# Performance work log

Measured on AMD Instinct MI355X. Metric: run time of the kernel, lower is better.

The kernel has to match this reference:

```python
import jax, jax.numpy as jnp
import numpy as np

DIM_M = 512
NEG_INF = -1e30


def setup_inputs() -> dict:
    key = jax.random.key(0)
    k1, k2, k3, k4, k5, k6, k7 = jax.random.split(key, 7)
    B, Lc, Lq, d = 16, 1024, 512, DIM_M
    C = jax.random.normal(k1, (B, Lc, d), dtype=jnp.float32)
    Q = jax.random.normal(k2, (B, Lq, d), dtype=jnp.float32)
    cmask = jax.random.randint(k3, (B, Lc), 0, 2).astype(jnp.float32)
    qmask = jax.random.randint(k4, (B, Lq), 0, 2).astype(jnp.float32)
    lim = np.sqrt(1.0 / d)
    w = jax.random.uniform(k5, (3 * d,), minval=-lim, maxval=lim, dtype=jnp.float32)
    # out_linear: Linear(4d -> d), torch default init
    bound = np.sqrt(1.0 / (4 * d))
    out_w = jax.random.uniform(k6, (d, 4 * d), minval=-bound, maxval=bound, dtype=jnp.float32)
    out_b = jax.random.uniform(k7, (d,), minval=-bound, maxval=bound, dtype=jnp.float32)
    return {"C": C, "Q": Q, "cmask": cmask, "qmask": qmask, "w": w, "out_w": out_w, "out_b": out_b}


def _mask_logits(t, m):
    return t * m + (1.0 - m) * NEG_INF


def reference(C, Q, cmask, qmask, w, out_w, out_b):
    d = C.shape[-1]
    w1, w2, w3 = w[:d], w[d:2 * d], w[2 * d:]
    # Decomposed trilinear similarity (same math as cat([Ct,Qt,Ct*Qt]) @ w):
    # S[b,i,j] = C[b,i]@w1 + Q[b,j]@w2 + (C[b,i]*w3) @ Q[b,j]
    S = (C @ w1)[:, :, None] + (Q @ w2)[:, None, :] \
        + jnp.einsum('bid,bjd->bij', C * w3, Q)  # [B, Lc, Lq]
    qm = qmask[:, None, :]  # [B, 1, Lq]
    cm = cmask[:, :, None]  # [B, Lc, 1]
    S1 = jax.nn.softmax(_mask_logits(S, qm), axis=2)  # over Lq
    S2 = jax.nn.softmax(_mask_logits(S, cm), axis=1)  # over Lc
    A = jnp.einsum('bij,bjd->bid', S1, Q)  # [B, Lc, d]
    # bmm(bmm(S1, S2^T), C) == S1 @ (S2^T @ C) by associativity (cheaper)
    S2TC = jnp.einsum('bij,bid->bjd', S2, C)  # [B, Lq, d]
    Bm = jnp.einsum('bij,bjd->bid', S1, S2TC)  # [B, Lc, d]
    out = jnp.concatenate([C, A, C * A, C * Bm], axis=2)  # [B, Lc, 4d]
    # dropout inactive (inference); out_linear
    return out @ out_w.T + out_b
```

## Files before the change

kernel.cpp:

```cpp
#include <hip/hip_runtime.h>
#include <hip/hip_bf16.h>


#define NB 16
#define LC 1024
#define LQ 512
#define DM 512
#define D4 2048
#define NEGINF (-1e30f)

typedef __bf16 v8bf __attribute__((ext_vector_type(8)));
typedef __bf16 v4bf __attribute__((ext_vector_type(4)));
typedef float  v4f  __attribute__((ext_vector_type(4)));

#define MFMA16 __builtin_amdgcn_mfma_f32_16x16x32_bf16

#define GLOAD16(gp, lp) __builtin_amdgcn_global_load_lds( \
    (const __attribute__((address_space(1))) void*)(gp), \
    (__attribute__((address_space(3))) void*)(lp), 16, 0, 0)

#define GEMM_PROLOG \
  __shared__ __bf16 Al[2][128 * 64], Bl[2][128 * 64]; \
  int bx = blockIdx.x, by = blockIdx.y, bz = blockIdx.z; \
  xcd_remap(bx, by, bz); \
  const int b = bz, i0 = by * 128, n0 = bx * 128; \
  const int t = threadIdx.x, lane = t & 63, wave = t >> 6; \
  const int wm = wave >> 1, wn = wave & 1, quad = lane >> 4, col = lane & 15; \
  const int srow = wave * 32 + (lane >> 3), scol = (lane & 7) * 8; \
  v4f acc[4][4]; \
  _Pragma("unroll") for (int x = 0; x < 4; ++x) \
  _Pragma("unroll") for (int y = 0; y < 4; ++y) \
  _Pragma("unroll") for (int r = 0; r < 4; ++r) acc[x][y][r] = 0.f;

#define GEMM_STAGE(buf, Aptr, Bptr, LDGA, LDGB, k0) \
  do { _Pragma("unroll") for (int u = 0; u < 4; ++u) { \
    GLOAD16((Aptr) + (size_t)(u * 8) * (LDGA) + (k0), &Al[buf][(wave * 32 + u * 8) * 64]); \
    GLOAD16((Bptr) + (size_t)(u * 8) * (LDGB) + (k0), &Bl[buf][(wave * 32 + u * 8) * 64]); \
  } } while (0)

#define GEMM_COMPUTE(buf) \
  do { _Pragma("unroll") for (int ko = 0; ko < 2; ++ko) { \
    v8bf af_[4], bf_[4]; \
    _Pragma("unroll") for (int x = 0; x < 4; ++x) \
      af_[x] = *(const v8bf*)&Al[buf][(wm * 64 + x * 16 + col) * 64 + ko * 32 + quad * 8]; \
    _Pragma("unroll") for (int y = 0; y < 4; ++y) \
      bf_[y] = *(const v8bf*)&Bl[buf][(wn * 64 + y * 16 + col) * 64 + ko * 32 + quad * 8]; \
    _Pragma("unroll") for (int x = 0; x < 4; ++x) \
    _Pragma("unroll") for (int y = 0; y < 4; ++y) \
      acc[x][y] = MFMA16(af_[x], bf_[y], acc[x][y], 0, 0, 0); \
  } } while (0)

#define GEMM_SYNC() \
  do { asm volatile("s_waitcnt vmcnt(0)" ::: "memory"); \
       __builtin_amdgcn_s_barrier(); } while (0)

#define GEMM_KLOOP(Arow, Brow, LDGA, LDGB, KEXT) \
  { GEMM_STAGE(0, Arow, Brow, LDGA, LDGB, 0); \
    GEMM_SYNC(); \
    int cur_ = 0; \
    for (int k0 = 0; k0 < (KEXT); k0 += 64) { \
      const int kn_ = k0 + 64; \
      if (kn_ < (KEXT)) GEMM_STAGE(cur_ ^ 1, Arow, Brow, LDGA, LDGB, kn_); \
      GEMM_COMPUTE(cur_); \
      GEMM_SYNC(); \
      cur_ ^= 1; \
    } }

__device__ __forceinline__ void xcd_remap(int& bx, int& by, int& bz) {
  const int gx = gridDim.x, gy = gridDim.y, gz = gridDim.z;
  int flat = bx + gx * (by + gy * bz);
  int per = (gx * gy * gz) >> 3;
  int nw = (flat & 7) * per + (flat >> 3);
  bx = nw % gx;
  int r = nw / gx;
  by = r % gy;
  bz = r / gy;
}

__global__ void k_rowdots(const float* __restrict__ C, const float* __restrict__ Q,
                          const float* __restrict__ w,
                          float* __restrict__ cw1, float* __restrict__ qw2,
                          __bf16* __restrict__ Cbf, __bf16* __restrict__ Qw3) {
  const int wid = threadIdx.x >> 6, lane = threadIdx.x & 63;
  const int row = blockIdx.x * 4 + wid;
  const bool isC = row < NB * LC;
  const int lr = isC ? row : row - NB * LC;
  const float* src = (isC ? C : Q) + (size_t)lr * DM;
  const float* wv  = isC ? w : (w + DM);
  const float* w3  = w + 2 * DM;
  __bf16* dst = (isC ? Cbf : Qw3) + (size_t)lr * DM;
  float v = 0.f;
#pragma unroll
  for (int s = 0; s < 2; ++s) {
    const int k = lane * 4 + s * 256;
    float4 f = *(const float4*)(src + k);
    float4 g = *(const float4*)(wv + k);
    v += f.x * g.x + f.y * g.y + f.z * g.z + f.w * g.w;
    v4bf h;
    if (isC) {
      h[0] = (__bf16)f.x; h[1] = (__bf16)f.y; h[2] = (__bf16)f.z; h[3] = (__bf16)f.w;
    } else {
      float4 s3 = *(const float4*)(w3 + k);
      h[0] = (__bf16)(f.x * s3.x); h[1] = (__bf16)(f.y * s3.y);
      h[2] = (__bf16)(f.z * s3.z); h[3] = (__bf16)(f.w * s3.w);
    }
    *(v4bf*)(dst + k) = h;
  }
#pragma unroll
  for (int off = 32; off; off >>= 1) v += __shfl_down(v, off, 64);
  if (lane == 0) {
    if (isC) cw1[row] = v;
    else     qw2[lr] = v;
  }
}

__global__ void k_transpose(const float* __restrict__ in, __bf16* __restrict__ outT,
                            int R, int Cd) {
  __shared__ __bf16 tile[64][66];
  const int b = blockIdx.z;
  const int r0 = blockIdx.y * 64, c0 = blockIdx.x * 64;
  const int tr = threadIdx.x >> 6, tc = threadIdx.x & 63;
  const float* inb = in + (size_t)b * R * Cd;
  __bf16* outb = outT + (size_t)b * Cd * R;
  for (int r = tr; r < 64; r += 4)
    tile[r][tc] = (__bf16)inb[(size_t)(r0 + r) * Cd + c0 + tc];
  __syncthreads();
  for (int c = tr; c < 64; c += 4)
    outb[(size_t)(c0 + c) * R + r0 + tc] = tile[tc][c];
}

__global__ void k_cvt2(const float* __restrict__ Cf, const float* __restrict__ OW,
                       __bf16* __restrict__ Cb3, __bf16* __restrict__ OWb) {
  const size_t NC = (size_t)NB * LC * DM;
  size_t i = ((size_t)blockIdx.x * 256 + threadIdx.x) * 4;
  const float* src; __bf16* dst; size_t j;
  if (i < NC) { src = Cf; dst = Cb3; j = i; }
  else        { src = OW; dst = OWb; j = i - NC; }
  float4 f = *(const float4*)(src + j);
  v4bf h; h[0] = (__bf16)f.x; h[1] = (__bf16)f.y; h[2] = (__bf16)f.z; h[3] = (__bf16)f.w;
  *(v4bf*)(dst + j) = h;
}

__global__ __launch_bounds__(256) void k_mfma_S(
    const __bf16* __restrict__ Cbf, const __bf16* __restrict__ Qw3,
    const float* __restrict__ cw1, const float* __restrict__ qw2,
    float* __restrict__ S) {
  GEMM_PROLOG
  const __bf16* Arow = Cbf + (size_t)b * LC * DM + (size_t)(i0 + srow) * DM + scol;
  const __bf16* Brow = Qw3 + (size_t)b * LQ * DM + (size_t)(n0 + srow) * DM + scol;
  GEMM_KLOOP(Arow, Brow, DM, DM, DM)
  float* Sb = S + (size_t)b * LC * LQ;
#pragma unroll
  for (int x = 0; x < 4; ++x) {
    const int mB = i0 + wm * 64 + x * 16 + quad * 4;
    float cv[4];
#pragma unroll
    for (int r = 0; r < 4; ++r) cv[r] = cw1[b * LC + mB + r];
#pragma unroll
    for (int y = 0; y < 4; ++y) {
      const int j = n0 + wn * 64 + y * 16 + col;
      const float qv = qw2[b * LQ + j];
#pragma unroll
      for (int r = 0; r < 4; ++r)
        Sb[(size_t)(mB + r) * LQ + j] = acc[x][y][r] + cv[r] + qv;
    }
  }
}

__global__ __launch_bounds__(1024) void k_softstat(
    const float* __restrict__ S, const float* __restrict__ qmask,
    const float* __restrict__ cmask, __bf16* __restrict__ S1,
    float2* __restrict__ pstat) {
  __shared__ float2 cst[16][LQ];
  const int b = blockIdx.y, ic = blockIdx.x;
  const int tid = threadIdx.x, wv = tid >> 6, lane = tid & 63;
  const float* qm  = qmask + b * LQ;
  const float* cm  = cmask + b * LC + ic * 64;
  const float* Sb  = S  + ((size_t)b * LC + ic * 64) * LQ;
  __bf16*      S1b = S1 + ((size_t)b * LC + ic * 64) * LQ;
  float colm[8], cols[8];
#pragma unroll
  for (int tt = 0; tt < 8; ++tt) { colm[tt] = -3e38f; cols[tt] = 0.f; }
  for (int it = 0; it < 4; ++it) {
    const int r = wv * 4 + it;
    const float cmv = cm[r];
    const float* Srow = Sb + (size_t)r * LQ;
    float sv[8], l1[8];
    float m = -3e38f;
#pragma unroll
    for (int tt = 0; tt < 8; ++tt) {
      int j = lane + 64 * tt;
      sv[tt] = Srow[j];
      float qv = qm[j];
      l1[tt] = qv * sv[tt] + (1.f - qv) * NEGINF;
      m = fmaxf(m, l1[tt]);
    }
#pragma unroll
    for (int off = 32; off; off >>= 1) m = fmaxf(m, __shfl_xor(m, off, 64));
    float e[8], s = 0.f;
#pragma unroll
    for (int tt = 0; tt < 8; ++tt) { e[tt] = __expf(l1[tt] - m); s += e[tt]; }
#pragma unroll
    for (int off = 32; off; off >>= 1) s += __shfl_xor(s, off, 64);
    const float inv = 1.f / s;
#pragma unroll
    for (int tt = 0; tt < 8; ++tt)
      S1b[(size_t)r * LQ + lane + 64 * tt] = (__bf16)(e[tt] * inv);
    if (cmv != 0.f) {
#pragma unroll
      for (int tt = 0; tt < 8; ++tt) {
        float l2 = sv[tt];
        if (l2 > colm[tt]) { cols[tt] *= __expf(colm[tt] - l2); colm[tt] = l2; }
        cols[tt] += __expf(l2 - colm[tt]);
      }
    }
  }
#pragma unroll
  for (int tt = 0; tt < 8; ++tt) cst[wv][lane + 64 * tt] = make_float2(colm[tt], cols[tt]);
  __syncthreads();
  if (tid < LQ) {
    float M = -3e38f, Sd = 0.f;
#pragma unroll
    for (int k = 0; k < 16; ++k) {
      float2 p = cst[k][tid];
      float nM = fmaxf(M, p.x);
      Sd = Sd * __expf(M - nM) + p.y * __expf(p.x - nM);
      M = nM;
    }
    pstat[((size_t)(b * 16 + ic) * LQ) + tid] = make_float2(M, Sd);
  }
}

__global__ void k_colwrite(const float* __restrict__ S, const float* __restrict__ cmask,
                           const float2* __restrict__ pstat, __bf16* __restrict__ S2T) {
  __shared__ float Mf[64], If[64];
  __shared__ __bf16 tile[64][66];
  const int b = blockIdx.z, ic = blockIdx.y, j0 = blockIdx.x * 64;
  const int c = threadIdx.x & 63, ip = threadIdx.x >> 6;
  if (threadIdx.x < 64) {
    float M = -3e38f, Sd = 0.f;
#pragma unroll
    for (int k = 0; k < 16; ++k) {
      float2 p = pstat[((size_t)(b * 16 + k) * LQ) + j0 + threadIdx.x];
      float nM = fmaxf(M, p.x);
      Sd = Sd * __expf(M - nM) + p.y * __expf(p.x - nM);
      M = nM;
    }
    Mf[threadIdx.x] = M; If[threadIdx.x] = 1.f / Sd;
  }
  __syncthreads();
  const float M = Mf[c], inv = If[c];
  const float* Sb = S + ((size_t)b * LC + ic * 64) * LQ;
  const float* cm = cmask + b * LC + ic * 64;
  for (int r = ip; r < 64; r += 4) {
    if (cm[r] != 0.f)
      tile[r][c] = (__bf16)(__expf(Sb[(size_t)r * LQ + j0 + c] - M) * inv);
    else
      tile[r][c] = (__bf16)0.f;
  }
  __syncthreads();
  __bf16* S2Tb = S2T + ((size_t)b * LQ + j0) * LC + ic * 64;
  for (int jr = ip; jr < 64; jr += 4)
    S2Tb[(size_t)jr * LC + c] = tile[c][jr];
}

__global__ __launch_bounds__(256) void k_mfma_A(
    const __bf16* __restrict__ S1, const __bf16* __restrict__ QT,
    const float* __restrict__ Cf, __bf16* __restrict__ Aw, __bf16* __restrict__ CAw) {
  GEMM_PROLOG
  const __bf16* Arow = S1 + (size_t)b * LC * LQ + (size_t)(i0 + srow) * LQ + scol;
  const __bf16* Brow = QT + (size_t)b * DM * LQ + (size_t)(n0 + srow) * LQ + scol;
  GEMM_KLOOP(Arow, Brow, LQ, LQ, LQ)
  const float* Cb = Cf + (size_t)b * LC * DM;
  __bf16* Ab  = Aw  + (size_t)b * LC * DM;
  __bf16* CAb = CAw + (size_t)b * LC * DM;
#pragma unroll
  for (int x = 0; x < 4; ++x) {
    const int mB = i0 + wm * 64 + x * 16 + quad * 4;
#pragma unroll
    for (int y = 0; y < 4; ++y) {
      const int n = n0 + wn * 64 + y * 16 + col;
#pragma unroll
      for (int r = 0; r < 4; ++r) {
        const float av = acc[x][y][r];
        const float cv = Cb[(size_t)(mB + r) * DM + n];
        Ab[(size_t)(mB + r) * DM + n]  = (__bf16)av;
        CAb[(size_t)(mB + r) * DM + n] = (__bf16)(av * cv);
      }
    }
  }
}

__global__ __launch_bounds__(256) void k_mfma_T(
    const __bf16* __restrict__ S2T, const __bf16* __restrict__ CT, __bf16* __restrict__ S2TCT) {
  GEMM_PROLOG
  const int j0 = i0;
  const __bf16* Arow = S2T + (size_t)b * LQ * LC + (size_t)(j0 + srow) * LC + scol;
  const __bf16* Brow = CT  + (size_t)b * DM * LC + (size_t)(n0 + srow) * LC + scol;
  GEMM_KLOOP(Arow, Brow, LC, LC, LC)
#pragma unroll
  for (int x = 0; x < 4; ++x) {
    const int jB = j0 + wm * 64 + x * 16 + quad * 4;
#pragma unroll
    for (int y = 0; y < 4; ++y) {
      const int n = n0 + wn * 64 + y * 16 + col;
      v4bf h;
#pragma unroll
      for (int r = 0; r < 4; ++r) h[r] = (__bf16)acc[x][y][r];
      *(v4bf*)&S2TCT[((size_t)b * DM + n) * LQ + jB] = h;
    }
  }
}

__global__ __launch_bounds__(256) void k_mfma_Bm(
    const __bf16* __restrict__ S1, const __bf16* __restrict__ S2TCT,
    const float* __restrict__ Cf, __bf16* __restrict__ CBw) {
  GEMM_PROLOG
  const __bf16* Arow = S1    + (size_t)b * LC * LQ + (size_t)(i0 + srow) * LQ + scol;
  const __bf16* Brow = S2TCT + (size_t)b * DM * LQ + (size_t)(n0 + srow) * LQ + scol;
  GEMM_KLOOP(Arow, Brow, LQ, LQ, LQ)
  const float* Cb = Cf + (size_t)b * LC * DM;
  __bf16* CBb = CBw + (size_t)b * LC * DM;
#pragma unroll
  for (int x = 0; x < 4; ++x) {
    const int mB = i0 + wm * 64 + x * 16 + quad * 4;
#pragma unroll
    for (int y = 0; y < 4; ++y) {
      const int n = n0 + wn * 64 + y * 16 + col;
#pragma unroll
      for (int r = 0; r < 4; ++r) {
        const float cv = Cb[(size_t)(mB + r) * DM + n];
        CBb[(size_t)(mB + r) * DM + n] = (__bf16)(acc[x][y][r] * cv);
      }
    }
  }
}

__global__ __launch_bounds__(256) void k_mfma_out(
    const __bf16* __restrict__ Cb3, const __bf16* __restrict__ Aw,
    const __bf16* __restrict__ CAw, const __bf16* __restrict__ CBw,
    const __bf16* __restrict__ OWb, const float* __restrict__ ob,
    float* __restrict__ out) {
  GEMM_PROLOG
  const size_t rowoff = (size_t)b * LC * DM + (size_t)(i0 + srow) * DM + scol;
  const __bf16* As0 = Cb3 + rowoff;
  const __bf16* As1 = Aw  + rowoff;
  const __bf16* As2 = CAw + rowoff;
  const __bf16* As3 = CBw + rowoff;
  const __bf16* Brow0 = OWb + (size_t)(n0 + srow) * D4 + scol;
  GEMM_STAGE(0, As0, Brow0, DM, D4, 0);
  GEMM_SYNC();
  int cur_ = 0;
#pragma unroll
  for (int seg = 0; seg < 4; ++seg) {
    const __bf16* Arow  = (seg == 0) ? As0 : (seg == 1) ? As1 : (seg == 2) ? As2 : As3;
    const __bf16* Anext = (seg == 0) ? As1 : (seg == 1) ? As2 : As3;
    const __bf16* Brow  = Brow0 + seg * DM;
    const __bf16* Bnext = Brow0 + (seg < 3 ? seg + 1 : 3) * DM;
    for (int k0 = 0; k0 < DM; k0 += 64) {
      const int kn_ = k0 + 64;
      if (kn_ < DM)      GEMM_STAGE(cur_ ^ 1, Arow, Brow, DM, D4, kn_);
      else if (seg < 3)  GEMM_STAGE(cur_ ^ 1, Anext, Bnext, DM, D4, 0);
      GEMM_COMPUTE(cur_);
      GEMM_SYNC();
      cur_ ^= 1;
    }
  }
  float* outb = out + (size_t)b * LC * DM;
#pragma unroll
  for (int x = 0; x < 4; ++x) {
    const int mB = i0 + wm * 64 + x * 16 + quad * 4;
#pragma unroll
    for (int y = 0; y < 4; ++y) {
      const int n = n0 + wn * 64 + y * 16 + col;
      const float bv = ob[n];
#pragma unroll
      for (int r = 0; r < 4; ++r)
        outb[(size_t)(mB + r) * DM + n] = acc[x][y][r] + bv;
    }
  }
}

extern "C" void kernel_launch(void* const* d_in, const int* in_sizes, int n_in,
                              void* d_out, int out_size, void* d_ws, size_t ws_size,
                              hipStream_t stream) {
  const float* C     = (const float*)d_in[0];
  const float* Q     = (const float*)d_in[1];
  const float* cmask = (const float*)d_in[2];
  const float* qmask = (const float*)d_in[3];
  const float* w     = (const float*)d_in[4];
  const float* out_w = (const float*)d_in[5];
  const float* out_b = (const float*)d_in[6];
  float* out = (float*)d_out;

  char* base = (char*)d_ws;
  float*  cw1   = (float*)base;
  float*  qw2   = (float*)(base + 65536);
  char*   R     = base + 131072;
  float*  S     = (float*)R;
  __bf16* CT    = (__bf16*)R;
  __bf16* Aw    = (__bf16*)R;
  __bf16* QT    = (__bf16*)(R + (16u << 20));
  __bf16* CBw   = (__bf16*)(R + (16u << 20));
  __bf16* Cbf_e = (__bf16*)(R + (32u << 20));
  __bf16* S1    = (__bf16*)(R + (32u << 20));
  __bf16* Cbf3  = (__bf16*)(R + (32u << 20));
  __bf16* Qw3   = (__bf16*)(R + (48u << 20));
  __bf16* S2T   = (__bf16*)(R + (48u << 20));
  __bf16* CAw   = (__bf16*)(R + (48u << 20));
  float2* pstat = (float2*)(R + (64u << 20));
  __bf16* S2TCT = (__bf16*)(R + (64u << 20));
  __bf16* OWbf  = (__bf16*)(R + (64u << 20));
  (void)in_sizes; (void)n_in; (void)out_size; (void)ws_size;

  k_rowdots<<<(NB * LC + NB * LQ) / 4, 256, 0, stream>>>(C, Q, w, cw1, qw2, Cbf_e, Qw3);
  k_mfma_S<<<dim3(LQ / 128, LC / 128, NB), 256, 0, stream>>>(Cbf_e, Qw3, cw1, qw2, S);
  k_softstat<<<dim3(LC / 64, NB), 1024, 0, stream>>>(S, qmask, cmask, S1, pstat);
  k_colwrite<<<dim3(LQ / 64, LC / 64, NB), 256, 0, stream>>>(S, cmask, pstat, S2T);
  k_transpose<<<dim3(DM / 64, LC / 64, NB), 256, 0, stream>>>(C, CT, LC, DM);
  k_mfma_T<<<dim3(DM / 128, LQ / 128, NB), 256, 0, stream>>>(S2T, CT, S2TCT);
  k_transpose<<<dim3(DM / 64, LQ / 64, NB), 256, 0, stream>>>(Q, QT, LQ, DM);
  k_mfma_A<<<dim3(DM / 128, LC / 128, NB), 256, 0, stream>>>(S1, QT, C, Aw, CAw);
  k_mfma_Bm<<<dim3(DM / 128, LC / 128, NB), 256, 0, stream>>>(S1, S2TCT, C, CBw);
  k_cvt2<<<(NB * LC * DM + DM * D4) / 1024, 256, 0, stream>>>(C, out_w, Cbf3, OWbf);
  k_mfma_out<<<dim3(DM / 128, LC / 128, NB), 256, 0, stream>>>(Cbf3, Aw, CAw, CBw, OWbf, out_b, out);
}
```

Before: 279.8 us.

## Halve GEMM K-tile, fuse transposes and weight cast, reuse bf16 C

Shrinks the GEMM K-tile from 64 to 32, halving LDS per block, at the cost of twice as many barrier and load rounds. Merges the two transpose kernels and the out_w bf16 cast into a single prep kernel to cut launches. When the workspace is large enough, the bf16 copy of C made by the row-dot kernel is kept in a separate region and reused by the output GEMM, which skips the separate C conversion pass. The unused k_cvt2 now has an odd store expression.

```diff
diff --git a/kernel.cpp b/kernel.cpp
--- a/kernel.cpp
+++ b/kernel.cpp
@@ -20,35 +20,35 @@
     (__attribute__((address_space(3))) void*)(lp), 16, 0, 0)
 
 #define GEMM_PROLOG \
-  __shared__ __bf16 Al[2][128 * 64], Bl[2][128 * 64]; \
+  __shared__ __bf16 Al[2][128 * 32], Bl[2][128 * 32]; \
   int bx = blockIdx.x, by = blockIdx.y, bz = blockIdx.z; \
   xcd_remap(bx, by, bz); \
   const int b = bz, i0 = by * 128, n0 = bx * 128; \
   const int t = threadIdx.x, lane = t & 63, wave = t >> 6; \
   const int wm = wave >> 1, wn = wave & 1, quad = lane >> 4, col = lane & 15; \
-  const int srow = wave * 32 + (lane >> 3), scol = (lane & 7) * 8; \
+  const int srow = wave * 32 + (lane >> 2), scol = (lane & 3) * 8; \
   v4f acc[4][4]; \
   _Pragma("unroll") for (int x = 0; x < 4; ++x) \
   _Pragma("unroll") for (int y = 0; y < 4; ++y) \
   _Pragma("unroll") for (int r = 0; r < 4; ++r) acc[x][y][r] = 0.f;
 
 #define GEMM_STAGE(buf, Aptr, Bptr, LDGA, LDGB, k0) \
-  do { _Pragma("unroll") for (int u = 0; u < 4; ++u) { \
-    GLOAD16((Aptr) + (size_t)(u * 8) * (LDGA) + (k0), &Al[buf][(wave * 32 + u * 8) * 64]); \
-    GLOAD16((Bptr) + (size_t)(u * 8) * (LDGB) + (k0), &Bl[buf][(wave * 32 + u * 8) * 64]); \
+  do { _Pragma("unroll") for (int u = 0; u < 2; ++u) { \
+    GLOAD16((Aptr) + (size_t)(u * 16) * (LDGA) + (k0), &Al[buf][(wave * 32 + u * 16) * 32]); \
+    GLOAD16((Bptr) + (size_t)(u * 16) * (LDGB) + (k0), &Bl[buf][(wave * 32 + u * 16) * 32]); \
   } } while (0)
 
 #define GEMM_COMPUTE(buf) \
-  do { _Pragma("unroll") for (int ko = 0; ko < 2; ++ko) { \
+  do { \
     v8bf af_[4], bf_[4]; \
     _Pragma("unroll") for (int x = 0; x < 4; ++x) \
-      af_[x] = *(const v8bf*)&Al[buf][(wm * 64 + x * 16 + col) * 64 + ko * 32 + quad * 8]; \
+      af_[x] = *(const v8bf*)&Al[buf][(wm * 64 + x * 16 + col) * 32 + quad * 8]; \
     _Pragma("unroll") for (int y = 0; y < 4; ++y) \
-      bf_[y] = *(const v8bf*)&Bl[buf][(wn * 64 + y * 16 + col) * 64 + ko * 32 + quad * 8]; \
+      bf_[y] = *(const v8bf*)&Bl[buf][(wn * 64 + y * 16 + col) * 32 + quad * 8]; \
     _Pragma("unroll") for (int x = 0; x < 4; ++x) \
     _Pragma("unroll") for (int y = 0; y < 4; ++y) \
       acc[x][y] = MFMA16(af_[x], bf_[y], acc[x][y], 0, 0, 0); \
-  } } while (0)
+  } while (0)
 
 #define GEMM_SYNC() \
   do { asm volatile("s_waitcnt vmcnt(0)" ::: "memory"); \
@@ -58,8 +58,8 @@
   { GEMM_STAGE(0, Arow, Brow, LDGA, LDGB, 0); \
     GEMM_SYNC(); \
     int cur_ = 0; \
-    for (int k0 = 0; k0 < (KEXT); k0 += 64) { \
-      const int kn_ = k0 + 64; \
+    for (int k0 = 0; k0 < (KEXT); k0 += 32) { \
+      const int kn_ = k0 + 32; \
       if (kn_ < (KEXT)) GEMM_STAGE(cur_ ^ 1, Arow, Brow, LDGA, LDGB, kn_); \
       GEMM_COMPUTE(cur_); \
       GEMM_SYNC(); \
@@ -114,19 +114,37 @@
   }
 }
 
-__global__ void k_transpose(const float* __restrict__ in, __bf16* __restrict__ outT,
-                            int R, int Cd) {
+__device__ __forceinline__ void transpose_tile(const float* __restrict__ in,
+                                               __bf16* __restrict__ outT,
+                                               int R, int Cd, int tbx, int tby, int tb) {
   __shared__ __bf16 tile[64][66];
-  const int b = blockIdx.z;
-  const int r0 = blockIdx.y * 64, c0 = blockIdx.x * 64;
+  const int r0 = tby * 64, c0 = tbx * 64;
   const int tr = threadIdx.x >> 6, tc = threadIdx.x & 63;
-  const float* inb = in + (size_t)b * R * Cd;
-  __bf16* outb = outT + (size_t)b * Cd * R;
+  const float* inb = in + (size_t)tb * R * Cd;
+  __bf16* outb = outT + (size_t)tb * Cd * R;
   for (int r = tr; r < 64; r += 4)
     tile[r][tc] = (__bf16)inb[(size_t)(r0 + r) * Cd + c0 + tc];
   __syncthreads();
   for (int c = tr; c < 64; c += 4)
     outb[(size_t)(c0 + c) * R + r0 + tc] = tile[tc][c];
+}
+
+__global__ void k_prep(const float* __restrict__ C, const float* __restrict__ Q,
+                       const float* __restrict__ OW,
+                       __bf16* __restrict__ CT, __bf16* __restrict__ QT,
+                       __bf16* __restrict__ OWb) {
+  const int id = blockIdx.x;
+  if (id < 2048) {
+    transpose_tile(C, CT, LC, DM, id & 7, (id >> 3) & 15, id >> 7);
+  } else if (id < 3072) {
+    const int id2 = id - 2048;
+    transpose_tile(Q, QT, LQ, DM, id2 & 7, (id2 >> 3) & 7, id2 >> 6);
+  } else {
+    const size_t i = ((size_t)(id - 3072) * 256 + threadIdx.x) * 4;
+    float4 f = *(const float4*)(OW + i);
+    v4bf h; h[0] = (__bf16)f.x; h[1] = (__bf16)f.y; h[2] = (__bf16)f.z; h[3] = (__bf16)f.w;
+    *(v4bf*)(OWb + i) = h;
+  }
 }
 
 __global__ void k_cvt2(const float* __restrict__ Cf, const float* __restrict__ OW,
@@ -138,7 +156,23 @@
   else        { src = OW; dst = OWb; j = i - NC; }
   float4 f = *(const float4*)(src + j);
   v4bf h; h[0] = (__bf16)f.x; h[1] = (__bf16)f.y; h[2] = (__bf16)f.z; h[3] = (__bf16)f.w;
-  *(v4bf*)(dst + j) = h;
+  *(v4bf*)(OWb ? dst : dst + j - j) = h;
+}
+
+__global__ void k_cvt2b(const float* __restrict__ Cf, const float* __restrict__ OW,
+                        __bf16* __restrict__ Cb3, __bf16* __restrict__ OWb) {
+  const size_t NC = (size_t)NB * LC * DM;
+  size_t i = ((size_t)blockIdx.x * 256 + threadIdx.x) * 4;
+  if (i < NC) {
+    float4 f = *(const float4*)(Cf + i);
+    v4bf h; h[0] = (__bf16)f.x; h[1] = (__bf16)f.y; h[2] = (__bf16)f.z; h[3] = (__bf16)f.w;
+    *(v4bf*)(Cb3 + i) = h;
+  } else {
+    size_t j = i - NC;
+    float4 f = *(const float4*)(OW + j);
+    v4bf h; h[0] = (__bf16)f.x; h[1] = (__bf16)f.y; h[2] = (__bf16)f.z; h[3] = (__bf16)f.w;
+    *(v4bf*)(OWb + j) = h;
+  }
 }
 
 __global__ __launch_bounds__(256) void k_mfma_S(
@@ -357,8 +391,8 @@
     const __bf16* Anext = (seg == 0) ? As1 : (seg == 1) ? As2 : As3;
     const __bf16* Brow  = Brow0 + seg * DM;
     const __bf16* Bnext = Brow0 + (seg < 3 ? seg + 1 : 3) * DM;
-    for (int k0 = 0; k0 < DM; k0 += 64) {
-      const int kn_ = k0 + 64;
+    for (int k0 = 0; k0 < DM; k0 += 32) {
+      const int kn_ = k0 + 32;
       if (kn_ < DM)      GEMM_STAGE(cur_ ^ 1, Arow, Brow, DM, D4, kn_);
       else if (seg < 3)  GEMM_STAGE(cur_ ^ 1, Anext, Bnext, DM, D4, 0);
       GEMM_COMPUTE(cur_);
@@ -402,26 +436,37 @@
   __bf16* Aw    = (__bf16*)R;
   __bf16* QT    = (__bf16*)(R + (16u << 20));
   __bf16* CBw   = (__bf16*)(R + (16u << 20));
-  __bf16* Cbf_e = (__bf16*)(R + (32u << 20));
   __bf16* S1    = (__bf16*)(R + (32u << 20));
-  __bf16* Cbf3  = (__bf16*)(R + (32u << 20));
   __bf16* Qw3   = (__bf16*)(R + (48u << 20));
   __bf16* S2T   = (__bf16*)(R + (48u << 20));
   __bf16* CAw   = (__bf16*)(R + (48u << 20));
   float2* pstat = (float2*)(R + (64u << 20));
   __bf16* S2TCT = (__bf16*)(R + (64u << 20));
-  __bf16* OWbf  = (__bf16*)(R + (64u << 20));
-  (void)in_sizes; (void)n_in; (void)out_size; (void)ws_size;
-
-  k_rowdots<<<(NB * LC + NB * LQ) / 4, 256, 0, stream>>>(C, Q, w, cw1, qw2, Cbf_e, Qw3);
-  k_mfma_S<<<dim3(LQ / 128, LC / 128, NB), 256, 0, stream>>>(Cbf_e, Qw3, cw1, qw2, S);
+  (void)in_sizes; (void)n_in; (void)out_size;
+
+  const size_t need_big = 131072 + (90ull << 20);
+  const bool bigws = ws_size >= need_big;
+
+  __bf16 *Cbf, *Cbf3, *OWbf;
+  if (bigws) {
+    Cbf  = (__bf16*)(R + (72u << 20));
+    Cbf3 = Cbf;
+    OWbf = (__bf16*)(R + (88u << 20));
+  } else {
+    Cbf  = (__bf16*)(R + (32u << 20));
+    Cbf3 = (__bf16*)(R + (32u << 20));
+    OWbf = (__bf16*)(R + (64u << 20));
+  }
+
+  k_rowdots<<<(NB * LC + NB * LQ) / 4, 256, 0, stream>>>(C, Q, w, cw1, qw2, Cbf, Qw3);
+  k_mfma_S<<<dim3(LQ / 128, LC / 128, NB), 256, 0, stream>>>(Cbf, Qw3, cw1, qw2, S);
   k_softstat<<<dim3(LC / 64, NB), 1024, 0, stream>>>(S, qmask, cmask, S1, pstat);
   k_colwrite<<<dim3(LQ / 64, LC / 64, NB), 256, 0, stream>>>(S, cmask, pstat, S2T);
-  k_transpose<<<dim3(DM / 64, LC / 64, NB), 256, 0, stream>>>(C, CT, LC, DM);
+  k_prep<<<bigws ? 4096 : 3072, 256, 0, stream>>>(C, Q, out_w, CT, QT, OWbf);
   k_mfma_T<<<dim3(DM / 128, LQ / 128, NB), 256, 0, stream>>>(S2T, CT, S2TCT);
-  k_transpose<<<dim3(DM / 64, LQ / 64, NB), 256, 0, stream>>>(Q, QT, LQ, DM);
   k_mfma_A<<<dim3(DM / 128, LC / 128, NB), 256, 0, stream>>>(S1, QT, C, Aw, CAw);
   k_mfma_Bm<<<dim3(DM / 128, LC / 128, NB), 256, 0, stream>>>(S1, S2TCT, C, CBw);
-  k_cvt2<<<(NB * LC * DM + DM * D4) / 1024, 256, 0, stream>>>(C, out_w, Cbf3, OWbf);
+  if (!bigws)
+    k_cvt2b<<<(NB * LC * DM + DM * D4) / 1024, 256, 0, stream>>>(C, out_w, Cbf3, OWbf);
   k_mfma_out<<<dim3(DM / 128, LC / 128, NB), 256, 0, stream>>>(Cbf3, Aw, CAw, CBw, OWbf, out_b, out);
 }
```

Result: no change. 285.2 us (+1.9%).
